# Optimization experiments

Hardware: AMD Instinct MI355X
Metric: run time of the kernel (lower is better)

The kernel has to match this reference:

```python
import jax, jax.numpy as jnp
import numpy as np

NUM_HEADS = 10
NEG_BIG = -2.0**32 + 1.0  # padding value used before softmax in the original
MASK_ADDER = -10000.0     # additive directional mask value


def setup_inputs() -> dict:
    key = jax.random.key(0)
    k1, k2, k3, k4, k5 = jax.random.split(key, 5)
    B, T, D, U = 8, 1024, 640, 640
    x = jax.random.normal(k1, (B, T, D), dtype=jnp.float32)
    mask = jax.random.randint(k2, (B, T), 0, 2, dtype=jnp.int32)
    s = 1.0 / np.sqrt(D)
    Wq = jax.random.normal(k3, (D, U), dtype=jnp.float32) * s
    Wk = jax.random.normal(k4, (D, U), dtype=jnp.float32) * s
    Wv = jax.random.normal(k5, (D, U), dtype=jnp.float32) * s
    return {"x": x, "mask": mask, "Wq": Wq, "Wk": Wk, "Wv": Wv}


def reference(x, mask, Wq, Wk, Wv):
    B, T, _ = x.shape
    H = NUM_HEADS
    U = Wq.shape[1]
    d = U // H

    # projections (no bias)
    Q = x @ Wq  # [B,T,U]
    K = x @ Wk
    V = x @ Wv

    # tf split(axis=2)+concat(axis=0) == head-major layout [H,B,T,d]
    def to_heads(t):
        return t.reshape(B, T, H, d).transpose(2, 0, 1, 3)

    Qh, Kh, Vh = to_heads(Q), to_heads(K), to_heads(V)

    scores = jnp.einsum('hbqd,hbkd->hbqk', Qh, Kh) / jnp.sqrt(jnp.float32(d))

    # key padding mask: sign(sum|K|) per key position
    key_m = jnp.sign(jnp.sum(jnp.abs(Kh), axis=-1))  # [H,B,T]
    scores = jnp.where(key_m[:, :, None, :] == 0, jnp.float32(NEG_BIG), scores)

    # directional mask: 'forward' -> attend strictly to past (row > col)
    row = jnp.arange(T)[:, None]
    col = jnp.arange(T)[None, :]
    allowed = (row > col).astype(scores.dtype)  # [T,T]
    scores = scores + (1.0 - allowed) * MASK_ADDER

    attn = jax.nn.softmax(scores, axis=-1)

    # post-softmax multiplicative query mask
    query_m = jnp.sign(jnp.sum(jnp.abs(Qh), axis=-1))  # [H,B,T]
    attn = attn * query_m[:, :, :, None]

    out = jnp.einsum('hbqk,hbkd->hbqd', attn, Vh)  # [H,B,T,d]
    out = out.transpose(1, 2, 0, 3).reshape(B, T, U)  # concat heads back on feature dim

    out = out * mask[:, :, None].astype(jnp.float32)
    return out
```

## Files before the change

### kernel.cpp

```cpp
#include <hip/hip_runtime.h>
#include <hip/hip_bf16.h>
#include <stdint.h>

#define B_DIM 8
#define T_DIM 1024
#define D_DIM 640
#define H_DIM 10
#define LOG2E 1.442695041f

typedef unsigned short ushort_t;
typedef __attribute__((ext_vector_type(8))) short short8;
typedef __attribute__((ext_vector_type(4))) float f32x4;
typedef __attribute__((ext_vector_type(16))) float f32x16;
typedef __attribute__((ext_vector_type(4))) unsigned int u32x4;

__device__ __forceinline__ ushort_t f32_to_bf16(float f) {
    unsigned int u = __builtin_bit_cast(unsigned int, f);
    u += 0x7fffu + ((u >> 16) & 1u);
    return (ushort_t)(u >> 16);
}
__device__ __forceinline__ float v_exp2(float x) {
    float r; asm("v_exp_f32 %0, %1" : "=v"(r) : "v"(x)); return r;
}
__device__ __forceinline__ unsigned cvt_pk_bf16(float a, float b) {
    unsigned r; asm("v_cvt_pk_bf16_f32 %0, %1, %2" : "=v"(r) : "v"(a), "v"(b)); return r;
}
__device__ __forceinline__ void gload16(const void* g, void* l) {
    auto gp = reinterpret_cast<const __attribute__((address_space(1))) uint32_t*>(
        reinterpret_cast<uintptr_t>(g));
    auto lp = reinterpret_cast<__attribute__((address_space(3))) uint32_t*>(
        reinterpret_cast<uintptr_t>(l));
    __builtin_amdgcn_global_load_lds(gp, lp, 16, 0, 0);
}

__constant__ int SPERM[32] = {0,31,30,29,28,27,26,25,24,23,22,21,20,19,18,17,
                              16,15,14,13,12,11,10,9,8,7,6,5,4,3,2,1};

__global__ __launch_bounds__(256) void convwt(
    const float* __restrict__ x,
    const float* __restrict__ Wq, const float* __restrict__ Wk, const float* __restrict__ Wv,
    ushort_t* __restrict__ xb, ushort_t* __restrict__ Wt)
{
    const int tid = threadIdx.x;
    if (blockIdx.x < 300) {
        const int w = blockIdx.x / 100, rem = blockIdx.x % 100;
        const int k0 = (rem % 10) * 64, n0 = (rem / 10) * 64;
        const float* W = (w == 0) ? Wq : (w == 1) ? Wk : Wv;
        ushort_t* Wo = Wt + (size_t)w * D_DIM * D_DIM;

        __shared__ alignas(16) ushort_t st[64][72];
        const int r = tid >> 2, cs = (tid & 3) * 16;
        #pragma unroll
        for (int j = 0; j < 4; ++j) {
            float4 v = *reinterpret_cast<const float4*>(
                &W[(size_t)(k0 + r) * D_DIM + n0 + cs + j * 4]);
            st[r][cs + j * 4 + 0] = f32_to_bf16(v.x);
            st[r][cs + j * 4 + 1] = f32_to_bf16(v.y);
            st[r][cs + j * 4 + 2] = f32_to_bf16(v.z);
            st[r][cs + j * 4 + 3] = f32_to_bf16(v.w);
        }
        __syncthreads();
        const int nr = tid >> 2, ks = (tid & 3) * 16;
        ushort_t tmp[16];
        #pragma unroll
        for (int j = 0; j < 16; ++j) tmp[j] = st[ks + j][nr];
        ushort_t* dst = &Wo[(size_t)(n0 + nr) * D_DIM + k0 + ks];
        *reinterpret_cast<short8*>(dst)     = *reinterpret_cast<const short8*>(&tmp[0]);
        *reinterpret_cast<short8*>(dst + 8) = *reinterpret_cast<const short8*>(&tmp[8]);
    } else {
        const int n8 = (B_DIM * T_DIM * D_DIM) / 8;
        for (int i = (blockIdx.x - 300) * 256 + tid; i < n8; i += 2048 * 256) {
            float4 a = *reinterpret_cast<const float4*>(&x[i * 8]);
            float4 b = *reinterpret_cast<const float4*>(&x[i * 8 + 4]);
            ushort_t o[8] = {f32_to_bf16(a.x), f32_to_bf16(a.y), f32_to_bf16(a.z), f32_to_bf16(a.w),
                             f32_to_bf16(b.x), f32_to_bf16(b.y), f32_to_bf16(b.z), f32_to_bf16(b.w)};
            *reinterpret_cast<short8*>(&xb[i * 8]) = *reinterpret_cast<const short8*>(o);
        }
    }
}

__global__ __launch_bounds__(256) void gemm_qkv(
    const ushort_t* __restrict__ xb, const ushort_t* __restrict__ Wt,
    const int* __restrict__ msk,
    ushort_t* __restrict__ QF, ushort_t* __restrict__ KF, ushort_t* __restrict__ VF,
    float* __restrict__ qs, ushort_t* __restrict__ km16)
{
    const int L = blockIdx.x;
    const int xcd = L & 7, j = L >> 3;
    const int m0 = (xcd * 8 + (j & 7)) * 128;
    const int nz = j >> 3;
    const int n0 = (nz % 5) * 128;
    const int w  = nz / 5;

    const ushort_t* Wm = Wt + (size_t)w * D_DIM * D_DIM;

    __shared__ alignas(16) ushort_t As[128 * 64];
    __shared__ alignas(16) ushort_t Bs[128 * 64];

    const int tid = threadIdx.x;
    const int lane = tid & 63, wave = tid >> 6;
    const int lo = lane & 15, g = lane >> 4;
    const int wm = wave >> 1, wn = wave & 1;
    const int srow = tid >> 3, schunk = tid & 7;

    f32x4 acc[4][4];
    #pragma unroll
    for (int i = 0; i < 4; ++i)
        #pragma unroll
        for (int jj = 0; jj < 4; ++jj) acc[i][jj] = (f32x4){0.f, 0.f, 0.f, 0.f};

    for (int k0 = 0; k0 < D_DIM; k0 += 64) {
        #pragma unroll
        for (int i = 0; i < 4; ++i) {
            int row = i * 32 + srow;
            int sc = schunk ^ (row & 7);
            gload16(&xb[(size_t)(m0 + row) * D_DIM + k0 + sc * 8], &As[i * 2048 + tid * 8]);
            gload16(&Wm[(size_t)(n0 + row) * D_DIM + k0 + sc * 8], &Bs[i * 2048 + tid * 8]);
        }
        __syncthreads();
        #pragma unroll
        for (int ks = 0; ks < 2; ++ks) {
            short8 af[4], bf[4];
            #pragma unroll
            for (int t = 0; t < 4; ++t) {
                int arow = wm * 64 + t * 16 + lo;
                int ach = (ks * 4 + g) ^ (arow & 7);
                af[t] = *reinterpret_cast<const short8*>(&As[arow * 64 + ach * 8]);
                int brow = wn * 64 + t * 16 + lo;
                int bch = (ks * 4 + g) ^ (brow & 7);
                bf[t] = *reinterpret_cast<const short8*>(&Bs[brow * 64 + bch * 8]);
            }
            __builtin_amdgcn_s_setprio(1);
            #pragma unroll
            for (int mi = 0; mi < 4; ++mi)
                #pragma unroll
                for (int ni = 0; ni < 4; ++ni)
                    acc[mi][ni] = __builtin_amdgcn_mfma_f32_16x16x32_bf16(
                        af[mi], bf[ni], acc[mi][ni], 0, 0, 0);
            __builtin_amdgcn_s_setprio(0);
        }
        __syncthreads();
    }

    const int hh = (n0 >> 6) + wn;
    const int bb = m0 >> 10;
    const int hb = hh * 8 + bb;
    const int ktw = ((m0 & 1023) >> 6) + wm;

    if (w == 2) {
        const int hiv = g >> 1, jj0 = (g & 1) * 4;
        #pragma unroll
        for (int mi = 0; mi < 4; ++mi)
            #pragma unroll
            for (int ni = 0; ni < 4; ++ni) {
                const int df = ni >> 1, l31v = (ni & 1) * 16 + lo;
                size_t idx = ((((size_t)(hb * 16 + ktw) * 4 + mi) * 2 + df) * 64
                              + hiv * 32 + l31v) * 8 + jj0;
                ushort4 o = make_ushort4(f32_to_bf16(acc[mi][ni][0]), f32_to_bf16(acc[mi][ni][1]),
                                         f32_to_bf16(acc[mi][ni][2]), f32_to_bf16(acc[mi][ni][3]));
                *reinterpret_cast<ushort4*>(&VF[idx]) = o;
            }
    } else {
        #pragma unroll
        for (int mi = 0; mi < 4; ++mi)
            #pragma unroll
            for (int r = 0; r < 4; ++r) {
                float s_ = fabsf(acc[mi][0][r]) + fabsf(acc[mi][1][r])
                         + fabsf(acc[mi][2][r]) + fabsf(acc[mi][3][r]);
                #pragma unroll
                for (int m = 1; m < 16; m <<= 1) s_ += __shfl_xor(s_, m);
                if (lo == 0) {
                    int row = m0 + wm * 64 + mi * 16 + g * 4 + r;
                    int rowid = hh * 8192 + row;
                    if (w == 0) qs[rowid] = (s_ > 0.f ? 1.f : 0.f) * (float)msk[row];
                    else        km16[rowid] = (s_ > 0.f) ? (ushort_t)0x3F80 : (ushort_t)0;
                }
            }
        const int hi2 = lo >> 3, jjq = lo & 7;
        const int s32base = ((m0 & 1023) + wm * 64) >> 5;
        #pragma unroll
        for (int mi = 0; mi < 4; ++mi)
            #pragma unroll
            for (int ni = 0; ni < 4; ++ni)
                #pragma unroll
                for (int r = 0; r < 4; ++r) {
                    int l31 = (mi & 1) * 16 + g * 4 + r;
                    if (w == 0) {
                        int s32 = s32base + (mi >> 1);
                        size_t idx = (((size_t)(hb * 32 + s32) * 4 + ni) * 64
                                      + hi2 * 32 + l31) * 8 + jjq;
                        QF[idx] = f32_to_bf16(acc[mi][ni][r]);
                    } else {
                        int f = (mi >> 1) & 1;
                        size_t idx = ((((size_t)(hb * 16 + ktw) * 2 + f) * 4 + ni) * 64
                                      + hi2 * 32 + l31) * 8 + jjq;
                        KF[idx] = f32_to_bf16(acc[mi][ni][r]);
                    }
                }
    }
}

#define DO_TILE(KT_IDX) do {                                                     \
    const int k0_ = (KT_IDX) * 64;                                               \
    const ushort_t* KT_ = &KFh[(size_t)(KT_IDX) * 4096];                         \
    const ushort_t* VT_ = &VFh[(size_t)(KT_IDX) * 4096];                         \
    short8 kA_[2][4];                                                            \
    _Pragma("unroll")                                                            \
    for (int f_ = 0; f_ < 2; ++f_)                                               \
        _Pragma("unroll")                                                        \
        for (int kc_ = 0; kc_ < 4; ++kc_)                                        \
            kA_[f_][kc_] = *reinterpret_cast<const short8*>(                     \
                &KT_[(f_ * 4 + kc_) * 512 + lane * 8]);                          \
    short8 vfA_[2][2], vfB_[2][2];                                               \
    _Pragma("unroll")                                                            \
    for (int c_ = 0; c_ < 2; ++c_)                                               \
        _Pragma("unroll")                                                        \
        for (int df_ = 0; df_ < 2; ++df_)                                        \
            vfA_[c_][df_] = *reinterpret_cast<const short8*>(                    \
                &VT_[(c_ * 2 + df_) * 512 + lane * 8]);                          \
    ushort4 kq_[2][4];                                                           \
    _Pragma("unroll")                                                            \
    for (int f_ = 0; f_ < 2; ++f_)                                               \
        _Pragma("unroll")                                                        \
        for (int rr_ = 0; rr_ < 4; ++rr_)                                        \
            kq_[f_][rr_] = *reinterpret_cast<const ushort4*>(                    \
                &kmr[k0_ + f_ * 32 + rr_ * 8 + hi * 4]);                         \
    unsigned pk_[2][8];                                                          \
    _Pragma("unroll")                                                            \
    for (int f_ = 0; f_ < 2; ++f_) {                                             \
        f32x16 sf_;                                                              \
        _Pragma("unroll")                                                        \
        for (int i_ = 0; i_ < 16; ++i_) sf_[i_] = 0.f;                           \
        __builtin_amdgcn_s_setprio(1);                                           \
        _Pragma("unroll")                                                        \
        for (int kc_ = 0; kc_ < 4; ++kc_)                                        \
            sf_ = __builtin_amdgcn_mfma_f32_32x32x16_bf16(kA_[f_][kc_],          \
                                                          qf[kc_], sf_, 0, 0, 0);\
        __builtin_amdgcn_s_setprio(0);                                           \
        if (f_ == 0) {                                                           \
            _Pragma("unroll")                                                    \
            for (int c_ = 0; c_ < 2; ++c_)                                       \
                _Pragma("unroll")                                                \
                for (int df_ = 0; df_ < 2; ++df_)                                \
                    vfB_[c_][df_] = *reinterpret_cast<const short8*>(            \
                        &VT_[((c_ + 2) * 2 + df_) * 512 + lane * 8]);            \
        }                                                                        \
        _Pragma("unroll")                                                        \
        for (int rr_ = 0; rr_ < 4; ++rr_) {                                      \
            const int kbase_ = k0_ + f_ * 32 + rr_ * 8 + hi * 4;                 \
            const ushort_t* kmv_ =                                               \
                reinterpret_cast<const ushort_t*>(&kq_[f_][rr_]);                \
            float p_[4];                                                         \
            _Pragma("unroll")                                                    \
            for (int ri_ = 0; ri_ < 4; ++ri_) {                                  \
                float cc_ = (kbase_ + ri_ >= trow) ? cB : cA;                    \
                cc_ = kmv_[ri_] ? cc_ : -1e30f;                                  \
                p_[ri_] = v_exp2(fmaf(sf_[rr_ * 4 + ri_], S2, cc_));             \
                lacc += p_[ri_];                                                 \
            }                                                                    \
            pk_[f_][rr_ * 2 + 0] = cvt_pk_bf16(p_[0], p_[1]);                    \
            pk_[f_][rr_ * 2 + 1] = cvt_pk_bf16(p_[2], p_[3]);                    \
        }                                                                        \
    }                                                                            \
    _Pragma("unroll")                                                            \
    for (int c_ = 0; c_ < 4; ++c_) {                                             \
        const int f_ = c_ >> 1, o_ = (c_ & 1) * 4;                               \
        unsigned a0_ = pk_[f_][o_ + 0], b0_ = pk_[f_][o_ + 2];                   \
        unsigned a1_ = pk_[f_][o_ + 1], b1_ = pk_[f_][o_ + 3];                   \
        if (v1) {                                                                \
            asm volatile("v_permlane32_swap_b32 %0, %1" : "+v"(b0_), "+v"(a0_)); \
            asm volatile("v_permlane32_swap_b32 %0, %1" : "+v"(b1_), "+v"(a1_)); \
        } else {                                                                 \
            asm volatile("v_permlane32_swap_b32 %0, %1" : "+v"(a0_), "+v"(b0_)); \
            asm volatile("v_permlane32_swap_b32 %0, %1" : "+v"(a1_), "+v"(b1_)); \
        }                                                                        \
        u32x4 pau_ = {a0_, a1_, b0_, b1_};                                       \
        short8 pa_ = __builtin_bit_cast(short8, pau_);                           \
        short8 v0_ = (c_ < 2) ? vfA_[c_][0] : vfB_[c_ - 2][0];                   \
        short8 v1f_ = (c_ < 2) ? vfA_[c_][1] : vfB_[c_ - 2][1];                  \
        __builtin_amdgcn_s_setprio(1);                                           \
        of0 = __builtin_amdgcn_mfma_f32_32x32x16_bf16(pa_, v0_, of0, 0, 0, 0);   \
        of1 = __builtin_amdgcn_mfma_f32_32x32x16_bf16(pa_, v1f_, of1, 0, 0, 0);  \
        __builtin_amdgcn_s_setprio(0);                                           \
    }                                                                            \
} while (0)

__global__ __launch_bounds__(256, 3) void attn_strip(
    const ushort_t* __restrict__ QF, const ushort_t* __restrict__ KF,
    const ushort_t* __restrict__ VF, const float* __restrict__ qs,
    const ushort_t* __restrict__ km16, float* __restrict__ out)
{
    __shared__ alignas(16) float mrg[3 * 64 * 36];

    const int tid = threadIdx.x, lane = tid & 63, wave = tid >> 6;
    const int l31 = lane & 31, hi = lane >> 5;

    const int bid = blockIdx.x;
    const int xcd = bid & 7, i = bid >> 3;
    const int sr = i / 10, grp = i % 10;
    const int g8 = xcd + 8 * grp;
    const int s = SPERM[sr], q0 = s * 32;
    const int b = g8 & 7, h = g8 >> 3, hb = h * 8 + b;

    unsigned pva = (unsigned)lane, pvb = 64u + (unsigned)lane;
    asm volatile("v_permlane32_swap_b32 %0, %1" : "+v"(pva), "+v"(pvb));
    const bool v1 = (__builtin_amdgcn_readfirstlane((int)pva) >= 96);

    const ushort_t* QFh = QF + (size_t)(hb * 32 + s) * 2048;
    const ushort_t* KFh = KF + (size_t)hb * 16 * 4096;
    const ushort_t* VFh = VF + (size_t)hb * 16 * 4096;
    const ushort_t* kmr = km16 + (size_t)hb * 1024;

    short8 qf[4];
    #pragma unroll
    for (int kc = 0; kc < 4; ++kc)
        qf[kc] = *reinterpret_cast<const short8*>(&QFh[kc * 512 + lane * 8]);

    bool anyPrior = false;
    for (int c = 0; c < (q0 >> 6); ++c) {
        ushort_t v = kmr[c * 64 + lane];
        anyPrior = anyPrior || (__ballot(v != 0) != 0ull);
    }
    float M;
    {
        ushort_t v = kmr[(q0 & ~63) + lane];
        unsigned long long bal = __ballot(v != 0);
        unsigned long long pre = bal & ((1ull << ((q0 & 63) + l31)) - 1ull);
        M = (anyPrior || pre != 0ull) ? 16.f : -9984.f;
    }
    const float cA = -M * LOG2E;
    const float cB = cA - 10000.0f * LOG2E;
    const float S2 = 0.125f * LOG2E;
    const int trow = q0 + l31;

    float lacc = 0.f;
    f32x16 of0, of1;
    #pragma unroll
    for (int i2 = 0; i2 < 16; ++i2) { of0[i2] = 0.f; of1[i2] = 0.f; }

    const int ktend = (s == 0) ? 16 : ((s >> 1) + 1);

    for (int kt = wave; kt < ktend; kt += 4)
        DO_TILE(kt);

    if (wave != 0) {
        float* dst = &mrg[((wave - 1) * 64 + lane) * 36];
        #pragma unroll
        for (int q = 0; q < 4; ++q) {
            reinterpret_cast<float4*>(dst)[q] =
                make_float4(of0[q * 4 + 0], of0[q * 4 + 1], of0[q * 4 + 2], of0[q * 4 + 3]);
            reinterpret_cast<float4*>(dst)[4 + q] =
                make_float4(of1[q * 4 + 0], of1[q * 4 + 1], of1[q * 4 + 2], of1[q * 4 + 3]);
        }
        dst[32] = lacc;
    }
    __syncthreads();
    if (wave == 0) {
        #pragma unroll
        for (int w2 = 0; w2 < 3; ++w2) {
            const float* src = &mrg[(w2 * 64 + lane) * 36];
            #pragma unroll
            for (int q = 0; q < 4; ++q) {
                float4 t0 = reinterpret_cast<const float4*>(src)[q];
                of0[q * 4 + 0] += t0.x; of0[q * 4 + 1] += t0.y;
                of0[q * 4 + 2] += t0.z; of0[q * 4 + 3] += t0.w;
                float4 t1 = reinterpret_cast<const float4*>(src)[4 + q];
                of1[q * 4 + 0] += t1.x; of1[q * 4 + 1] += t1.y;
                of1[q * 4 + 2] += t1.z; of1[q * 4 + 3] += t1.w;
            }
            lacc += src[32];
        }
        float ltot = lacc + __shfl_xor(lacc, 32);
        float scale = qs[(size_t)hb * 1024 + q0 + l31] / ltot;
        const size_t obase = ((size_t)b * T_DIM + q0) * D_DIM + h * 64;
        #pragma unroll
        for (int reg = 0; reg < 16; ++reg) {
            const int qrow = (reg & 3) + 8 * (reg >> 2) + 4 * hi;
            const float sc = __shfl(scale, qrow);
            out[obase + (size_t)qrow * D_DIM + l31]      = of0[reg] * sc;
            out[obase + (size_t)qrow * D_DIM + 32 + l31] = of1[reg] * sc;
        }
    }
}

extern "C" void kernel_launch(void* const* d_in, const int* in_sizes, int n_in,
                              void* d_out, int out_size, void* d_ws, size_t ws_size,
                              hipStream_t stream)
{
    const float* x   = (const float*)d_in[0];
    const int*   msk = (const int*)d_in[1];
    const float* Wq  = (const float*)d_in[2];
    const float* Wk  = (const float*)d_in[3];
    const float* Wv  = (const float*)d_in[4];
    float* out = (float*)d_out;

    char* ws = (char*)d_ws;
    ushort_t* xb = (ushort_t*)(ws);
    ushort_t* Wt = (ushort_t*)(ws + 10485760);
    ushort_t* QF = (ushort_t*)(ws + 12943360);
    ushort_t* KF = (ushort_t*)(ws + 23429120);
    ushort_t* VF = (ushort_t*)(ws + 33914880);
    float*    qs = (float*)(ws + 44400640);
    ushort_t* km = (ushort_t*)(ws + 44728320);
    if (ws_size < 44892160) return;

    convwt<<<2348, 256, 0, stream>>>(x, Wq, Wk, Wv, xb, Wt);
    gemm_qkv<<<960, 256, 0, stream>>>(xb, Wt, msk, QF, KF, VF, qs, km);
    attn_strip<<<2560, 256, 0, stream>>>(QF, KF, VF, qs, km, out);
}
```

Baseline: 79.18 us.

## Double-buffer QKV GEMM k-tiles and use ballot for row-nonzero masks

Result: no change. 78.05 us (-1.4%).

```diff
diff --git a/kernel.cpp b/kernel.cpp
--- a/kernel.cpp
+++ b/kernel.cpp
@@ -94,14 +94,13 @@
 
     const ushort_t* Wm = Wt + (size_t)w * D_DIM * D_DIM;
 
-    __shared__ alignas(16) ushort_t As[128 * 64];
-    __shared__ alignas(16) ushort_t Bs[128 * 64];
+    __shared__ alignas(16) ushort_t As[2][128 * 32];
+    __shared__ alignas(16) ushort_t Bs[2][128 * 32];
 
     const int tid = threadIdx.x;
     const int lane = tid & 63, wave = tid >> 6;
     const int lo = lane & 15, g = lane >> 4;
     const int wm = wave >> 1, wn = wave & 1;
-    const int srow = tid >> 3, schunk = tid & 7;
 
     f32x4 acc[4][4];
     #pragma unroll
@@ -109,38 +108,52 @@
         #pragma unroll
         for (int jj = 0; jj < 4; ++jj) acc[i][jj] = (f32x4){0.f, 0.f, 0.f, 0.f};
 
-    for (int k0 = 0; k0 < D_DIM; k0 += 64) {
-        #pragma unroll
-        for (int i = 0; i < 4; ++i) {
-            int row = i * 32 + srow;
-            int sc = schunk ^ (row & 7);
-            gload16(&xb[(size_t)(m0 + row) * D_DIM + k0 + sc * 8], &As[i * 2048 + tid * 8]);
-            gload16(&Wm[(size_t)(n0 + row) * D_DIM + k0 + sc * 8], &Bs[i * 2048 + tid * 8]);
-        }
-        __syncthreads();
-        #pragma unroll
-        for (int ks = 0; ks < 2; ++ks) {
-            short8 af[4], bf[4];
+#define GSTAGE(K0_, BUF_) do {                                                   \
+        _Pragma("unroll")                                                        \
+        for (int i_ = 0; i_ < 2; ++i_) {                                         \
+            int slot_ = i_ * 256 + tid;                                          \
+            int row_ = slot_ >> 2;                                               \
+            int sc_ = (slot_ & 3) ^ ((row_ >> 1) & 3);                           \
+            gload16(&xb[(size_t)(m0 + row_) * D_DIM + (K0_) + sc_ * 8],          \
+                    &As[BUF_][slot_ * 8]);                                       \
+            gload16(&Wm[(size_t)(n0 + row_) * D_DIM + (K0_) + sc_ * 8],          \
+                    &Bs[BUF_][slot_ * 8]);                                       \
+        }                                                                        \
+    } while (0)
+
+    GSTAGE(0, 0);
+    int cur = 0;
+    for (int it = 0; it < 20; ++it) {
+        if (it < 19) {
+            GSTAGE((it + 1) * 32, cur ^ 1);
+            asm volatile("s_waitcnt vmcnt(4)" ::: "memory");
+        } else {
+            asm volatile("s_waitcnt vmcnt(0)" ::: "memory");
+        }
+        __builtin_amdgcn_s_barrier();
+
+        short8 af[4], bf[4];
+        #pragma unroll
+        for (int t = 0; t < 4; ++t) {
+            int arow = wm * 64 + t * 16 + lo;
+            int ach = g ^ ((arow >> 1) & 3);
+            af[t] = *reinterpret_cast<const short8*>(&As[cur][(arow * 4 + ach) * 8]);
+            int brow = wn * 64 + t * 16 + lo;
+            int bch = g ^ ((brow >> 1) & 3);
+            bf[t] = *reinterpret_cast<const short8*>(&Bs[cur][(brow * 4 + bch) * 8]);
+        }
+        __builtin_amdgcn_s_setprio(1);
+        #pragma unroll
+        for (int mi = 0; mi < 4; ++mi)
             #pragma unroll
-            for (int t = 0; t < 4; ++t) {
-                int arow = wm * 64 + t * 16 + lo;
-                int ach = (ks * 4 + g) ^ (arow & 7);
-                af[t] = *reinterpret_cast<const short8*>(&As[arow * 64 + ach * 8]);
-                int brow = wn * 64 + t * 16 + lo;
-                int bch = (ks * 4 + g) ^ (brow & 7);
-                bf[t] = *reinterpret_cast<const short8*>(&Bs[brow * 64 + bch * 8]);
-            }
-            __builtin_amdgcn_s_setprio(1);
-            #pragma unroll
-            for (int mi = 0; mi < 4; ++mi)
-                #pragma unroll
-                for (int ni = 0; ni < 4; ++ni)
-                    acc[mi][ni] = __builtin_amdgcn_mfma_f32_16x16x32_bf16(
-                        af[mi], bf[ni], acc[mi][ni], 0, 0, 0);
-            __builtin_amdgcn_s_setprio(0);
-        }
-        __syncthreads();
-    }
+            for (int ni = 0; ni < 4; ++ni)
+                acc[mi][ni] = __builtin_amdgcn_mfma_f32_16x16x32_bf16(
+                    af[mi], bf[ni], acc[mi][ni], 0, 0, 0);
+        __builtin_amdgcn_s_setprio(0);
+        __builtin_amdgcn_s_barrier();
+        cur ^= 1;
+    }
+#undef GSTAGE
 
     const int hh = (n0 >> 6) + wn;
     const int bb = m0 >> 10;
@@ -167,13 +180,13 @@
             for (int r = 0; r < 4; ++r) {
                 float s_ = fabsf(acc[mi][0][r]) + fabsf(acc[mi][1][r])
                          + fabsf(acc[mi][2][r]) + fabsf(acc[mi][3][r]);
-                #pragma unroll
-                for (int m = 1; m < 16; m <<= 1) s_ += __shfl_xor(s_, m);
+                unsigned long long bal = __ballot(s_ != 0.f);
                 if (lo == 0) {
                     int row = m0 + wm * 64 + mi * 16 + g * 4 + r;
                     int rowid = hh * 8192 + row;
-                    if (w == 0) qs[rowid] = (s_ > 0.f ? 1.f : 0.f) * (float)msk[row];
-                    else        km16[rowid] = (s_ > 0.f) ? (ushort_t)0x3F80 : (ushort_t)0;
+                    bool nz = ((bal >> (g * 16)) & 0xFFFFull) != 0ull;
+                    if (w == 0) qs[rowid] = (nz ? 1.f : 0.f) * (float)msk[row];
+                    else        km16[rowid] = nz ? (ushort_t)0x3F80 : (ushort_t)0;
                 }
             }
         const int hi2 = lo >> 3, jjq = lo & 7;
```

## Pre-swizzle x and W into MFMA fragment layout and drop LDS staging in QKV GEMM

Applied to the files above, without the earlier changes.

Measured after the change: 121.0 us. 52.8% more time.

```diff
diff --git a/kernel.cpp b/kernel.cpp
--- a/kernel.cpp
+++ b/kernel.cpp
@@ -25,28 +25,21 @@
 __device__ __forceinline__ unsigned cvt_pk_bf16(float a, float b) {
     unsigned r; asm("v_cvt_pk_bf16_f32 %0, %1, %2" : "=v"(r) : "v"(a), "v"(b)); return r;
 }
-__device__ __forceinline__ void gload16(const void* g, void* l) {
-    auto gp = reinterpret_cast<const __attribute__((address_space(1))) uint32_t*>(
-        reinterpret_cast<uintptr_t>(g));
-    auto lp = reinterpret_cast<__attribute__((address_space(3))) uint32_t*>(
-        reinterpret_cast<uintptr_t>(l));
-    __builtin_amdgcn_global_load_lds(gp, lp, 16, 0, 0);
-}
 
 __constant__ int SPERM[32] = {0,31,30,29,28,27,26,25,24,23,22,21,20,19,18,17,
                               16,15,14,13,12,11,10,9,8,7,6,5,4,3,2,1};
+
 
 __global__ __launch_bounds__(256) void convwt(
     const float* __restrict__ x,
     const float* __restrict__ Wq, const float* __restrict__ Wk, const float* __restrict__ Wv,
-    ushort_t* __restrict__ xb, ushort_t* __restrict__ Wt)
+    ushort_t* __restrict__ XF, ushort_t* __restrict__ WF)
 {
     const int tid = threadIdx.x;
     if (blockIdx.x < 300) {
         const int w = blockIdx.x / 100, rem = blockIdx.x % 100;
         const int k0 = (rem % 10) * 64, n0 = (rem / 10) * 64;
         const float* W = (w == 0) ? Wq : (w == 1) ? Wk : Wv;
-        ushort_t* Wo = Wt + (size_t)w * D_DIM * D_DIM;
 
         __shared__ alignas(16) ushort_t st[64][72];
         const int r = tid >> 2, cs = (tid & 3) * 16;
@@ -60,48 +53,64 @@
             st[r][cs + j * 4 + 3] = f32_to_bf16(v.w);
         }
         __syncthreads();
-        const int nr = tid >> 2, ks = (tid & 3) * 16;
-        ushort_t tmp[16];
-        #pragma unroll
-        for (int j = 0; j < 16; ++j) tmp[j] = st[ks + j][nr];
-        ushort_t* dst = &Wo[(size_t)(n0 + nr) * D_DIM + k0 + ks];
-        *reinterpret_cast<short8*>(dst)     = *reinterpret_cast<const short8*>(&tmp[0]);
-        *reinterpret_cast<short8*>(dst + 8) = *reinterpret_cast<const short8*>(&tmp[8]);
+        #pragma unroll
+        for (int q = 0; q < 2; ++q) {
+            int c = tid * 2 + q;
+            int fi = c >> 6, lane = c & 63;
+            int n16l = fi >> 1, kcl = fi & 1;
+            int nl = n16l * 16 + (lane & 15);
+            int klb = kcl * 32 + (lane >> 4) * 8;
+            ushort_t tmp[8];
+            #pragma unroll
+            for (int jj = 0; jj < 8; ++jj) tmp[jj] = st[klb + jj][nl];
+            size_t frag = ((size_t)w * 40 + (n0 >> 4) + n16l) * 20 + (k0 >> 5) + kcl;
+            *reinterpret_cast<short8*>(&WF[frag * 512 + lane * 8]) =
+                *reinterpret_cast<const short8*>(tmp);
+        }
     } else {
-        const int n8 = (B_DIM * T_DIM * D_DIM) / 8;
-        for (int i = (blockIdx.x - 300) * 256 + tid; i < n8; i += 2048 * 256) {
-            float4 a = *reinterpret_cast<const float4*>(&x[i * 8]);
-            float4 b = *reinterpret_cast<const float4*>(&x[i * 8 + 4]);
-            ushort_t o[8] = {f32_to_bf16(a.x), f32_to_bf16(a.y), f32_to_bf16(a.z), f32_to_bf16(a.w),
-                             f32_to_bf16(b.x), f32_to_bf16(b.y), f32_to_bf16(b.z), f32_to_bf16(b.w)};
-            *reinterpret_cast<short8*>(&xb[i * 8]) = *reinterpret_cast<const short8*>(o);
-        }
-    }
-}
-
-__global__ __launch_bounds__(256) void gemm_qkv(
-    const ushort_t* __restrict__ xb, const ushort_t* __restrict__ Wt,
+        const int mb = blockIdx.x - 300;
+        __shared__ alignas(16) ushort_t xt[16][132];
+        const int fl = tid * 2;
+        const int row = fl >> 5, c4 = fl & 31;
+        const int lane = tid & 63, wv = tid >> 6;
+        const int lo = lane & 15, g = lane >> 4;
+        #pragma unroll
+        for (int sl = 0; sl < 5; ++sl) {
+            const float* src = &x[((size_t)mb * 16 + row) * D_DIM + sl * 128 + c4 * 4];
+            float4 v0 = *reinterpret_cast<const float4*>(src);
+            float4 v1 = *reinterpret_cast<const float4*>(src + 4);
+            ushort_t o[8] = {f32_to_bf16(v0.x), f32_to_bf16(v0.y), f32_to_bf16(v0.z),
+                             f32_to_bf16(v0.w), f32_to_bf16(v1.x), f32_to_bf16(v1.y),
+                             f32_to_bf16(v1.z), f32_to_bf16(v1.w)};
+            *reinterpret_cast<short8*>(&xt[row][c4 * 4]) =
+                *reinterpret_cast<const short8*>(o);
+            __syncthreads();
+            short8 val = *reinterpret_cast<const short8*>(&xt[lo][wv * 32 + g * 8]);
+            *reinterpret_cast<short8*>(
+                &XF[(((size_t)mb * 20) + sl * 4 + wv) * 512 + lane * 8]) = val;
+            __syncthreads();
+        }
+    }
+}
+
+__global__ __launch_bounds__(256, 4) void gemm_qkv(
+    const ushort_t* __restrict__ XF, const ushort_t* __restrict__ WF,
     const int* __restrict__ msk,
     ushort_t* __restrict__ QF, ushort_t* __restrict__ KF, ushort_t* __restrict__ VF,
     float* __restrict__ qs, ushort_t* __restrict__ km16)
 {
-    const int L = blockIdx.x;
-    const int xcd = L & 7, j = L >> 3;
-    const int m0 = (xcd * 8 + (j & 7)) * 128;
-    const int nz = j >> 3;
-    const int n0 = (nz % 5) * 128;
-    const int w  = nz / 5;
-
-    const ushort_t* Wm = Wt + (size_t)w * D_DIM * D_DIM;
-
-    __shared__ alignas(16) ushort_t As[128 * 64];
-    __shared__ alignas(16) ushort_t Bs[128 * 64];
-
-    const int tid = threadIdx.x;
-    const int lane = tid & 63, wave = tid >> 6;
+    const int tid = threadIdx.x, lane = tid & 63, wave = tid >> 6;
     const int lo = lane & 15, g = lane >> 4;
-    const int wm = wave >> 1, wn = wave & 1;
-    const int srow = tid >> 3, schunk = tid & 7;
+    const int bid = blockIdx.x;
+    const int xcd = bid & 7;
+    const int gid = (bid >> 3) * 4 + wave;
+    const int w = gid / 160;
+    const int rem = gid - w * 160;
+    const int nt = rem >> 4;
+    const int mt = xcd * 16 + (rem & 15);
+
+    const ushort_t* XA = XF + (size_t)mt * 4 * 20 * 512;
+    const ushort_t* WB = WF + ((size_t)w * 40 + nt * 4) * 20 * 512;
 
     f32x4 acc[4][4];
     #pragma unroll
@@ -109,43 +118,51 @@
         #pragma unroll
         for (int jj = 0; jj < 4; ++jj) acc[i][jj] = (f32x4){0.f, 0.f, 0.f, 0.f};
 
-    for (int k0 = 0; k0 < D_DIM; k0 += 64) {
-        #pragma unroll
-        for (int i = 0; i < 4; ++i) {
-            int row = i * 32 + srow;
-            int sc = schunk ^ (row & 7);
-            gload16(&xb[(size_t)(m0 + row) * D_DIM + k0 + sc * 8], &As[i * 2048 + tid * 8]);
-            gload16(&Wm[(size_t)(n0 + row) * D_DIM + k0 + sc * 8], &Bs[i * 2048 + tid * 8]);
-        }
-        __syncthreads();
-        #pragma unroll
-        for (int ks = 0; ks < 2; ++ks) {
-            short8 af[4], bf[4];
-            #pragma unroll
-            for (int t = 0; t < 4; ++t) {
-                int arow = wm * 64 + t * 16 + lo;
-                int ach = (ks * 4 + g) ^ (arow & 7);
-                af[t] = *reinterpret_cast<const short8*>(&As[arow * 64 + ach * 8]);
-                int brow = wn * 64 + t * 16 + lo;
-                int bch = (ks * 4 + g) ^ (brow & 7);
-                bf[t] = *reinterpret_cast<const short8*>(&Bs[brow * 64 + bch * 8]);
-            }
-            __builtin_amdgcn_s_setprio(1);
-            #pragma unroll
-            for (int mi = 0; mi < 4; ++mi)
-                #pragma unroll
-                for (int ni = 0; ni < 4; ++ni)
-                    acc[mi][ni] = __builtin_amdgcn_mfma_f32_16x16x32_bf16(
-                        af[mi], bf[ni], acc[mi][ni], 0, 0, 0);
-            __builtin_amdgcn_s_setprio(0);
-        }
-        __syncthreads();
-    }
-
-    const int hh = (n0 >> 6) + wn;
-    const int bb = m0 >> 10;
+#define LDA(DST, KC) do {                                                        \
+        _Pragma("unroll")                                                        \
+        for (int i_ = 0; i_ < 4; ++i_)                                           \
+            DST[i_] = *reinterpret_cast<const short8*>(                          \
+                &XA[((size_t)(i_ * 20) + (KC)) * 512 + lane * 8]);               \
+    } while (0)
+#define LDB(DST, KC) do {                                                        \
+        _Pragma("unroll")                                                        \
+        for (int j_ = 0; j_ < 4; ++j_)                                           \
+            DST[j_] = *reinterpret_cast<const short8*>(                          \
+                &WB[((size_t)(j_ * 20) + (KC)) * 512 + lane * 8]);               \
+    } while (0)
+#define MM(AF, BF) do {                                                          \
+        __builtin_amdgcn_s_setprio(1);                                           \
+        _Pragma("unroll")                                                        \
+        for (int mi_ = 0; mi_ < 4; ++mi_)                                        \
+            _Pragma("unroll")                                                    \
+            for (int ni_ = 0; ni_ < 4; ++ni_)                                    \
+                acc[mi_][ni_] = __builtin_amdgcn_mfma_f32_16x16x32_bf16(         \
+                    AF[mi_], BF[ni_], acc[mi_][ni_], 0, 0, 0);                   \
+        __builtin_amdgcn_s_setprio(0);                                           \
+    } while (0)
+
+    short8 a0[4], a1[4], b0[4];
+    LDA(a0, 0);
+    #pragma unroll
+    for (int kc = 0; kc < 20; kc += 2) {
+        LDA(a1, kc + 1);
+        LDB(b0, kc);
+        MM(a0, b0);
+        if (kc + 2 < 20) LDA(a0, kc + 2);
+        LDB(b0, kc + 1);
+        MM(a1, b0);
+    }
+#undef LDA
+#undef LDB
+#undef MM
+
+    const int M0 = mt * 64;
+    const int N0 = nt * 64;
+    const int hh = nt;
+    const int bb = M0 >> 10;
     const int hb = hh * 8 + bb;
-    const int ktw = ((m0 & 1023) >> 6) + wm;
+    const int Mloc = M0 & 1023;
+    const int ktw = Mloc >> 6;
 
     if (w == 2) {
         const int hiv = g >> 1, jj0 = (g & 1) * 4;
@@ -167,17 +184,17 @@
             for (int r = 0; r < 4; ++r) {
                 float s_ = fabsf(acc[mi][0][r]) + fabsf(acc[mi][1][r])
                          + fabsf(acc[mi][2][r]) + fabsf(acc[mi][3][r]);
-                #pragma unroll
-                for (int m = 1; m < 16; m <<= 1) s_ += __shfl_xor(s_, m);
+                unsigned long long bal = __ballot(s_ != 0.f);
                 if (lo == 0) {
-                    int row = m0 + wm * 64 + mi * 16 + g * 4 + r;
+                    int row = M0 + mi * 16 + g * 4 + r;
                     int rowid = hh * 8192 + row;
-                    if (w == 0) qs[rowid] = (s_ > 0.f ? 1.f : 0.f) * (float)msk[row];
-                    else        km16[rowid] = (s_ > 0.f) ? (ushort_t)0x3F80 : (ushort_t)0;
+                    bool nz = ((bal >> (g * 16)) & 0xFFFFull) != 0ull;
+                    if (w == 0) qs[rowid] = (nz ? 1.f : 0.f) * (float)msk[row];
+                    else        km16[rowid] = nz ? (ushort_t)0x3F80 : (ushort_t)0;
                 }
             }
         const int hi2 = lo >> 3, jjq = lo & 7;
-        const int s32base = ((m0 & 1023) + wm * 64) >> 5;
+        const int s32base = Mloc >> 5;
         #pragma unroll
         for (int mi = 0; mi < 4; ++mi)
             #pragma unroll
@@ -395,8 +412,8 @@
     float* out = (float*)d_out;
 
     char* ws = (char*)d_ws;
-    ushort_t* xb = (ushort_t*)(ws);
-    ushort_t* Wt = (ushort_t*)(ws + 10485760);
+    ushort_t* XF = (ushort_t*)(ws);
+    ushort_t* WF = (ushort_t*)(ws + 10485760);
     ushort_t* QF = (ushort_t*)(ws + 12943360);
     ushort_t* KF = (ushort_t*)(ws + 23429120);
     ushort_t* VF = (ushort_t*)(ws + 33914880);
@@ -404,7 +421,7 @@
     ushort_t* km = (ushort_t*)(ws + 44728320);
     if (ws_size < 44892160) return;
 
-    convwt<<<2348, 256, 0, stream>>>(x, Wq, Wk, Wv, xb, Wt);
-    gemm_qkv<<<960, 256, 0, stream>>>(xb, Wt, msk, QF, KF, VF, qs, km);
+    convwt<<<812, 256, 0, stream>>>(x, Wq, Wk, Wv, XF, WF);
+    gemm_qkv<<<960, 256, 0, stream>>>(XF, WF, msk, QF, KF, VF, qs, km);
     attn_strip<<<2560, 256, 0, stream>>>(QF, KF, VF, qs, km, out);
 }
```
